# Kernel tuning notes

Hardware: AMD Instinct MI355X
Metric: run time of the kernel (lower is better)

The kernel has to match this reference:

```python
import jax, jax.numpy as jnp
import numpy as np

K = 3          # kernel size
DIL = 1        # dilation
PAD = (K + (K - 1) * (DIL - 1)) // 2   # = 1
CENTER = (K * K - 1) // 2              # = 4
D_MIN = 0.0
D_MAX = 10.0
MIN_NGHBR = 4


def _unfold(x):
    """x: (B,C,H,W) -> patches (B,H,W,k*k,C), matching torch.nn.Unfold ordering."""
    b, c, h, w = x.shape
    xp = jnp.pad(x, ((0, 0), (0, 0), (PAD, PAD), (PAD, PAD)))
    # fixed k*k=9 taps: loop over the kernel window only (not data dims)
    pats = [xp[:, :, i * DIL:i * DIL + h, j * DIL:j * DIL + w]
            for i in range(K) for j in range(K)]
    p = jnp.stack(pats, axis=2)          # (B,C,kk,H,W)
    return p.transpose(0, 3, 4, 2, 1)    # (B,H,W,kk,C)


def setup_inputs() -> dict:
    key = jax.random.key(0)
    kxy, kz = jax.random.split(key)
    B, H, W = 4, 480, 640
    xy = jax.random.normal(kxy, (B, 2, H, W), dtype=jnp.float32)
    z = jax.random.uniform(kz, (B, 1, H, W), dtype=jnp.float32, minval=0.1, maxval=9.9)
    points = jnp.concatenate([xy, z], axis=1)  # (B,3,H,W)
    return {"points": points}


def reference(points):
    b, _, h, w = points.shape
    # 3x3 neighborhoods of 3D points: (B,H,W,9,3)
    A3 = _unfold(points)
    # depth-validity mask, unfolded over the same window: (B,H,W,9,1)
    depth = points[:, 2:3]
    valid = ((depth > D_MIN) & (depth < D_MAX)).astype(points.dtype)
    vc = _unfold(valid)
    # homogeneous design matrix A = [x y z 1], zeroed where neighbor invalid
    A = jnp.concatenate([A3, jnp.ones_like(A3[..., :1])], axis=-1)  # (B,H,W,9,4)
    A = jnp.where(vc > 0.5, A, jnp.zeros_like(A))
    # normal equations: per-pixel symmetric PSD 4x4
    AtA = jnp.einsum('bhwki,bhwkj->bhwij', A, A)
    # A^T A is symmetric PSD -> real eigensystem; eigh gives ascending eigvals,
    # so the null-space direction (smallest eigval) is column 0.
    eig_val, eig_vec = jnp.linalg.eigh(AtA)
    normal4 = eig_vec[..., :, 0]                      # (B,H,W,4)
    normal = normal4[..., :3].transpose(0, 3, 1, 2)   # (B,3,H,W)
    # F.normalize(p=2, dim=1, eps=1e-12)
    nrm = jnp.linalg.norm(normal, axis=1, keepdims=True)
    normal = normal / jnp.maximum(nrm, 1e-12)
    # orient toward the camera ray
    flip = jnp.sign(jnp.sum(normal * points, axis=1, keepdims=True))
    normal = normal * flip
    # validity masks
    vm1 = vc[:, :, :, CENTER, 0][:, None] > 0.5                 # center pixel valid
    vm2 = jnp.sum(vc[..., 0], axis=3)[:, None] >= MIN_NGHBR    # enough neighbors
    # vm3 (real eigensystem) is always True for the symmetric solve
    vm4 = jnp.linalg.norm(normal, axis=1, keepdims=True) > 0.5
    valid_mask = vm1 & vm2 & vm4
    return normal, valid_mask
```

## Files before the change

### kernel.cpp

```cpp
#include <hip/hip_runtime.h>

#define BB 4
#define HH 480
#define WW 640

__device__ __forceinline__ double det3d(double a, double b, double c,
                                        double d, double e, double f,
                                        double g, double h, double i) {
    return a * (e * i - f * h) - b * (d * i - f * g) + c * (d * h - e * g);
}
__device__ __forceinline__ double sdet3d(double a, double b, double c,
                                         double e, double f, double i) {
    return a * (e * i - f * f) + b * (2.0 * c * f - b * i) - c * c * e;
}
__device__ __forceinline__ double crcp(double d) {
    return (double)__builtin_amdgcn_rcpf((float)d);
}
__device__ __forceinline__ float det3f(float a, float b, float c,
                                       float d, float e, float f,
                                       float g, float h, float i) {
    return a * (e * i - f * h) - b * (d * i - f * g) + c * (d * h - e * g);
}
__device__ __forceinline__ float sdet3f(float a, float b, float c,
                                        float e, float f, float i) {
    return a * (e * i - f * f) + b * (2.0f * c * f - b * i) - c * c * e;
}

__global__ __launch_bounds__(256) void d2n_kernel(const float* __restrict__ pts,
                                                  float* __restrict__ out) {
    int idx = blockIdx.x * 256 + threadIdx.x;
    if (idx >= BB * HH * WW) return;
    int x = idx % WW;
    int t1 = idx / WW;
    int y = t1 % HH;
    int b = t1 / HH;

    const size_t HW = (size_t)HH * WW;
    const float* xs = pts + ((size_t)b * 3 + 0) * HW;
    const float* ys = pts + ((size_t)b * 3 + 1) * HW;
    const float* zs = pts + ((size_t)b * 3 + 2) * HW;

    int row[3], col[3];
    bool rin[3], cin[3];
#pragma unroll
    for (int k = 0; k < 3; ++k) {
        int yy = y + k - 1, xx = x + k - 1;
        rin[k] = (unsigned)yy < HH;
        cin[k] = (unsigned)xx < WW;
        row[k] = min(max(yy, 0), HH - 1) * WW;
        col[k] = min(max(xx, 0), WW - 1);
    }
    float px[9], py[9], pz[9];
    bool inb[9];
#pragma unroll
    for (int i = 0; i < 9; ++i) {
        int r = i / 3, c = i % 3;
        int o = row[r] + col[c];
        inb[i] = rin[r] & cin[c];
        pz[i] = zs[o];
        px[i] = xs[o];
        py[i] = ys[o];
    }

    float sxx = 0.f, sxy = 0.f, sxz = 0.f, sx = 0.f;
    float syy = 0.f, syz = 0.f, sy = 0.f;
    float szz = 0.f, sz = 0.f, cnt = 0.f;
#pragma unroll
    for (int i = 0; i < 9; ++i) {
        float w = (inb[i] && pz[i] > 0.0f && pz[i] < 10.0f) ? 1.0f : 0.0f;
        float qx = px[i] * w, qy = py[i] * w, qz = pz[i] * w;
        sxx += qx * px[i]; sxy += qx * py[i]; sxz += qx * pz[i]; sx += qx;
        syy += qy * py[i]; syz += qy * pz[i]; sy += qy;
        szz += qz * pz[i]; sz += qz;
        cnt += w;
    }

    float trf = sxx + syy + szz + cnt;
    float itf = __builtin_amdgcn_rcpf(trf);
    float f00 = sxx * itf, f01 = sxy * itf, f02 = sxz * itf, f03 = sx * itf;
    float f11 = syy * itf, f12 = syz * itf, f13 = sy * itf;
    float f22 = szz * itf, f23 = sz * itf, f33 = cnt * itf;

    float e1f = f00 + f11 + f22 + f33;
    float e2f = (f00 * f11 - f01 * f01) + (f00 * f22 - f02 * f02) +
                (f00 * f33 - f03 * f03) + (f11 * f22 - f12 * f12) +
                (f11 * f33 - f13 * f13) + (f22 * f33 - f23 * f23);
    float Q0 = sdet3f(f11, f12, f13, f22, f23, f33);
    float Q1 = sdet3f(f00, f02, f03, f22, f23, f33);
    float Q2 = sdet3f(f00, f01, f03, f11, f13, f33);
    float Q3 = sdet3f(f00, f01, f02, f11, f12, f22);
    float e3f = Q0 + Q1 + Q2 + Q3;
    float e4f = f00 * Q0
              - f01 * det3f(f01, f12, f13, f02, f22, f23, f03, f23, f33)
              + f02 * det3f(f01, f11, f13, f02, f12, f23, f03, f13, f33)
              - f03 * det3f(f01, f11, f12, f02, f12, f22, f03, f13, f23);

    float t31f = 3.0f * e1f, t22f = 2.0f * e2f;
    float lf = 0.0f;
#pragma unroll
    for (int itn = 0; itn < 10; ++itn) {
        float p  = (((lf - e1f) * lf + e2f) * lf - e3f) * lf + e4f;
        float dp = ((4.0f * lf - t31f) * lf + t22f) * lf - e3f;
        dp = fminf(dp, -1e-30f);
        lf = lf - p * __builtin_amdgcn_rcpf(dp);
        lf = fminf(fmaxf(lf, 0.0f), 0.26f);
    }
    float dpf = ((4.0f * lf - t31f) * lf + t22f) * lf - e3f;

    float g0 = f00 - lf, g1 = f11 - lf, g2 = f22 - lf, g3 = f33 - lf;
    float B00 =  sdet3f(g1, f12, f13, g2, f23, g3);
    float B11 =  sdet3f(g0, f02, f03, g2, f23, g3);
    float B22 =  sdet3f(g0, f01, f03, g1, f13, g3);
    float B33 =  sdet3f(g0, f01, f02, g1, f12, g2);
    float B01 = -det3f(f01, f12, f13, f02, g2, f23, f03, f23, g3);
    float B02 =  det3f(f01, g1, f13, f02, f12, f23, f03, f13, g3);
    float B03 = -det3f(f01, g1, f12, f02, f12, g2, f03, f13, f23);
    float B12 = -det3f(g0, f01, f03, f02, f12, f23, f03, f13, g3);
    float B13 =  det3f(g0, f01, f02, f02, f12, g2, f03, f13, f23);
    float B23 = -det3f(g0, f01, f02, f01, g1, f12, f03, f13, f23);

    float bestf = fabsf(B00);
    float fx = B00, fy = B01, fz = B02;
    float b1a = fabsf(B11);
    if (b1a > bestf) { bestf = b1a; fx = B01; fy = B11; fz = B12; }
    float b2a = fabsf(B22);
    if (b2a > bestf) { bestf = b2a; fx = B02; fy = B12; fz = B22; }
    float b3a = fabsf(B33);
    if (b3a > bestf) { bestf = b3a; fx = B03; fy = B13; fz = B23; }

    float ndf = fx * fx + fy * fy + fz * fz;

    bool flag = !(dpf < -2e-4f) || (lf > 0.2599f) || !(ndf > 1e-12f);

    if (__any(flag)) {
        double tr = (double)sxx + (double)syy + (double)szz + (double)cnt;
        double it = crcp(tr);
        double m00 = sxx * it, m01 = sxy * it, m02 = sxz * it, m03 = sx * it;
        double m11 = syy * it, m12 = syz * it, m13 = sy * it;
        double m22 = szz * it, m23 = sz * it, m33 = cnt * it;

        double e1 = m00 + m11 + m22 + m33;
        double e2 = (m00 * m11 - m01 * m01) + (m00 * m22 - m02 * m02) +
                    (m00 * m33 - m03 * m03) + (m11 * m22 - m12 * m12) +
                    (m11 * m33 - m13 * m13) + (m22 * m33 - m23 * m23);
        double P0 = sdet3d(m11, m12, m13, m22, m23, m33);
        double P1 = sdet3d(m00, m02, m03, m22, m23, m33);
        double P2 = sdet3d(m00, m01, m03, m11, m13, m33);
        double P3 = sdet3d(m00, m01, m02, m11, m12, m22);
        double e3 = P0 + P1 + P2 + P3;
        double e4 = m00 * P0
                  - m01 * det3d(m01, m12, m13, m02, m22, m23, m03, m23, m33)
                  + m02 * det3d(m01, m11, m13, m02, m12, m23, m03, m13, m33)
                  - m03 * det3d(m01, m11, m12, m02, m12, m22, m03, m13, m23);

        double t31 = 3.0 * e1, t22 = 2.0 * e2;
        double lam = 0.0;
#pragma unroll
        for (int itn = 0; itn < 14; ++itn) {
            double p  = (((lam - e1) * lam + e2) * lam - e3) * lam + e4;
            double dp = ((4.0 * lam - t31) * lam + t22) * lam - e3;
            dp = fmin(dp, -1e-30);
            lam = lam - p * crcp(dp);
            lam = fmin(fmax(lam, 0.0), 0.26);
        }

        double d0 = m00 - lam, d1 = m11 - lam, d2 = m22 - lam, d3 = m33 - lam;
        double C00 =  sdet3d(d1, m12, m13, d2, m23, d3);
        double C11 =  sdet3d(d0, m02, m03, d2, m23, d3);
        double C22 =  sdet3d(d0, m01, m03, d1, m13, d3);
        double C33 =  sdet3d(d0, m01, m02, d1, m12, d2);
        double C01 = -det3d(m01, m12, m13, m02, d2, m23, m03, m23, d3);
        double C02 =  det3d(m01, d1, m13, m02, m12, m23, m03, m13, d3);
        double C03 = -det3d(m01, d1, m12, m02, m12, d2, m03, m13, m23);
        double C12 = -det3d(d0, m01, m03, m02, m12, m23, m03, m13, d3);
        double C13 =  det3d(d0, m01, m02, m02, m12, d2, m03, m13, m23);
        double C23 = -det3d(d0, m01, m02, m01, d1, m12, m03, m13, m23);

        double best = fabs(C00);
        double vx = C00, vy = C01, vz = C02, vd = C00;
        double a1 = fabs(C11);
        if (a1 > best) { best = a1; vx = C01; vy = C11; vz = C12; vd = C11; }
        double a2 = fabs(C22);
        if (a2 > best) { best = a2; vx = C02; vy = C12; vz = C22; vd = C22; }
        double a3 = fabs(C33);
        if (a3 > best) { best = a3; vx = C03; vy = C13; vz = C23; vd = C33; }

        double sc = crcp(vd);
        float gx = (float)(vx * sc), gy = (float)(vy * sc), gz = (float)(vz * sc);

        fx = flag ? gx : fx;
        fy = flag ? gy : fy;
        fz = flag ? gz : fz;
        ndf = fx * fx + fy * fy + fz * fz;
    }

    float inv = __builtin_amdgcn_rsqf(fmaxf(ndf, 1e-30f));
    float nx = fx * inv, ny = fy * inv, nz = fz * inv;

    int o = y * WW + x;
    float cx = px[4], cy = py[4], cz = pz[4];
    float dot = nx * cx + ny * cy + nz * cz;
    float sgn = (dot > 0.0f) ? 1.0f : ((dot < 0.0f) ? -1.0f : 0.0f);
    nx *= sgn; ny *= sgn; nz *= sgn;

    out[((size_t)b * 3 + 0) * HW + o] = nx;
    out[((size_t)b * 3 + 1) * HW + o] = ny;
    out[((size_t)b * 3 + 2) * HW + o] = nz;

    bool cvalid = (cz > 0.0f && cz < 10.0f);
    bool m = cvalid && (cnt >= 4.0f) && (nx * nx + ny * ny + nz * nz > 0.25f);
    out[(size_t)BB * 3 * HW + (size_t)b * HW + o] = m ? 1.0f : 0.0f;
}

extern "C" void kernel_launch(void* const* d_in, const int* in_sizes, int n_in,
                              void* d_out, int out_size, void* d_ws, size_t ws_size,
                              hipStream_t stream) {
    const float* pts = (const float*)d_in[0];
    float* out = (float*)d_out;
    int total = BB * HH * WW;
    d2n_kernel<<<(total + 255) / 256, 256, 0, stream>>>(pts, out);
}
```

Measured before the change: 96.87 us.

## Move double-precision fallback into a separate compacted fixup kernel

The main kernel now computes only the float eigenvector path and writes its result for every pixel. Pixels whose float solution looks unreliable are appended to a workspace list through a global atomic counter. A second kernel reloads their neighbourhoods, recomputes the normal in double precision and overwrites the output. This removes the wave-wide divergence where one flagged lane pulled the whole wavefront through the double path. The flag threshold is also loosened so fewer pixels go to the fallback. The cost is a memset, an extra launch, atomic contention on one counter, and possible accuracy loss from the looser threshold.

Result: slower. 206.2 us (+112.9%).

```diff
diff --git a/kernel.cpp b/kernel.cpp
--- a/kernel.cpp
+++ b/kernel.cpp
@@ -3,6 +3,7 @@
 #define BB 4
 #define HH 480
 #define WW 640
+#define NPIX (BB * HH * WW)
 
 __device__ __forceinline__ double det3d(double a, double b, double c,
                                         double d, double e, double f,
@@ -26,20 +27,15 @@
     return a * (e * i - f * f) + b * (2.0f * c * f - b * i) - c * c * e;
 }
 
-__global__ __launch_bounds__(256) void d2n_kernel(const float* __restrict__ pts,
-                                                  float* __restrict__ out) {
-    int idx = blockIdx.x * 256 + threadIdx.x;
-    if (idx >= BB * HH * WW) return;
-    int x = idx % WW;
-    int t1 = idx / WW;
-    int y = t1 % HH;
-    int b = t1 / HH;
-
+__device__ __forceinline__ void load_gram(const float* __restrict__ pts, int x, int y, int b,
+                                          float& sxx, float& sxy, float& sxz, float& sx,
+                                          float& syy, float& syz, float& sy,
+                                          float& szz, float& sz, float& cnt,
+                                          float& cx, float& cy, float& cz) {
     const size_t HW = (size_t)HH * WW;
     const float* xs = pts + ((size_t)b * 3 + 0) * HW;
     const float* ys = pts + ((size_t)b * 3 + 1) * HW;
     const float* zs = pts + ((size_t)b * 3 + 2) * HW;
-
     int row[3], col[3];
     bool rin[3], cin[3];
 #pragma unroll
@@ -61,10 +57,7 @@
         px[i] = xs[o];
         py[i] = ys[o];
     }
-
-    float sxx = 0.f, sxy = 0.f, sxz = 0.f, sx = 0.f;
-    float syy = 0.f, syz = 0.f, sy = 0.f;
-    float szz = 0.f, sz = 0.f, cnt = 0.f;
+    sxx = sxy = sxz = sx = syy = syz = sy = szz = sz = cnt = 0.f;
 #pragma unroll
     for (int i = 0; i < 9; ++i) {
         float w = (inb[i] && pz[i] > 0.0f && pz[i] < 10.0f) ? 1.0f : 0.0f;
@@ -74,6 +67,40 @@
         szz += qz * pz[i]; sz += qz;
         cnt += w;
     }
+    cx = px[4]; cy = py[4]; cz = pz[4];
+}
+
+__device__ __forceinline__ void finish_store(float* __restrict__ out, int x, int y, int b,
+                                             float fx, float fy, float fz,
+                                             float cx, float cy, float cz, float cnt) {
+    const size_t HW = (size_t)HH * WW;
+    float nd = fx * fx + fy * fy + fz * fz;
+    float inv = __builtin_amdgcn_rsqf(fmaxf(nd, 1e-30f));
+    float nx = fx * inv, ny = fy * inv, nz = fz * inv;
+    float dot = nx * cx + ny * cy + nz * cz;
+    float sgn = (dot > 0.0f) ? 1.0f : ((dot < 0.0f) ? -1.0f : 0.0f);
+    nx *= sgn; ny *= sgn; nz *= sgn;
+    int o = y * WW + x;
+    out[((size_t)b * 3 + 0) * HW + o] = nx;
+    out[((size_t)b * 3 + 1) * HW + o] = ny;
+    out[((size_t)b * 3 + 2) * HW + o] = nz;
+    bool cvalid = (cz > 0.0f && cz < 10.0f);
+    bool m = cvalid && (cnt >= 4.0f) && (nx * nx + ny * ny + nz * nz > 0.25f);
+    out[(size_t)BB * 3 * HW + (size_t)b * HW + o] = m ? 1.0f : 0.0f;
+}
+
+__global__ __launch_bounds__(256) void d2n_main(const float* __restrict__ pts,
+                                                float* __restrict__ out,
+                                                int* __restrict__ wslist, int cap) {
+    int idx = blockIdx.x * 256 + threadIdx.x;
+    if (idx >= NPIX) return;
+    int x = idx % WW;
+    int t1 = idx / WW;
+    int y = t1 % HH;
+    int b = t1 / HH;
+
+    float sxx, sxy, sxz, sx, syy, syz, sy, szz, sz, cnt, cx, cy, cz;
+    load_gram(pts, x, y, b, sxx, sxy, sxz, sx, syy, syz, sy, szz, sz, cnt, cx, cy, cz);
 
     float trf = sxx + syy + szz + cnt;
     float itf = __builtin_amdgcn_rcpf(trf);
@@ -130,9 +157,29 @@
 
     float ndf = fx * fx + fy * fy + fz * fz;
 
-    bool flag = !(dpf < -2e-4f) || (lf > 0.2599f) || !(ndf > 1e-12f);
-
-    if (__any(flag)) {
+    bool flag = !(dpf < -2e-5f) || (lf > 0.2599f) || !(ndf > 1e-12f);
+    if (flag) {
+        int slot = atomicAdd(wslist, 1);
+        if (slot < cap) wslist[1 + slot] = idx;
+    }
+
+    finish_store(out, x, y, b, fx, fy, fz, cx, cy, cz, cnt);
+}
+
+__global__ __launch_bounds__(256) void d2n_fixup(const float* __restrict__ pts,
+                                                 float* __restrict__ out,
+                                                 const int* __restrict__ wslist, int cap) {
+    int count = min(wslist[0], cap);
+    for (int i = blockIdx.x * 256 + threadIdx.x; i < count; i += gridDim.x * 256) {
+        int idx = wslist[1 + i];
+        int x = idx % WW;
+        int t1 = idx / WW;
+        int y = t1 % HH;
+        int b = t1 / HH;
+
+        float sxx, sxy, sxz, sx, syy, syz, sy, szz, sz, cnt, cx, cy, cz;
+        load_gram(pts, x, y, b, sxx, sxy, sxz, sx, syy, syz, sy, szz, sz, cnt, cx, cy, cz);
+
         double tr = (double)sxx + (double)syy + (double)szz + (double)cnt;
         double it = crcp(tr);
         double m00 = sxx * it, m01 = sxy * it, m02 = sxz * it, m03 = sx * it;
@@ -186,30 +233,10 @@
         if (a3 > best) { best = a3; vx = C03; vy = C13; vz = C23; vd = C33; }
 
         double sc = crcp(vd);
-        float gx = (float)(vx * sc), gy = (float)(vy * sc), gz = (float)(vz * sc);
-
-        fx = flag ? gx : fx;
-        fy = flag ? gy : fy;
-        fz = flag ? gz : fz;
-        ndf = fx * fx + fy * fy + fz * fz;
-    }
-
-    float inv = __builtin_amdgcn_rsqf(fmaxf(ndf, 1e-30f));
-    float nx = fx * inv, ny = fy * inv, nz = fz * inv;
-
-    int o = y * WW + x;
-    float cx = px[4], cy = py[4], cz = pz[4];
-    float dot = nx * cx + ny * cy + nz * cz;
-    float sgn = (dot > 0.0f) ? 1.0f : ((dot < 0.0f) ? -1.0f : 0.0f);
-    nx *= sgn; ny *= sgn; nz *= sgn;
-
-    out[((size_t)b * 3 + 0) * HW + o] = nx;
-    out[((size_t)b * 3 + 1) * HW + o] = ny;
-    out[((size_t)b * 3 + 2) * HW + o] = nz;
-
-    bool cvalid = (cz > 0.0f && cz < 10.0f);
-    bool m = cvalid && (cnt >= 4.0f) && (nx * nx + ny * ny + nz * nz > 0.25f);
-    out[(size_t)BB * 3 * HW + (size_t)b * HW + o] = m ? 1.0f : 0.0f;
+        float fx = (float)(vx * sc), fy = (float)(vy * sc), fz = (float)(vz * sc);
+
+        finish_store(out, x, y, b, fx, fy, fz, cx, cy, cz, cnt);
+    }
 }
 
 extern "C" void kernel_launch(void* const* d_in, const int* in_sizes, int n_in,
@@ -217,6 +244,10 @@
                               hipStream_t stream) {
     const float* pts = (const float*)d_in[0];
     float* out = (float*)d_out;
-    int total = BB * HH * WW;
-    d2n_kernel<<<(total + 255) / 256, 256, 0, stream>>>(pts, out);
-}
+    int* wslist = (int*)d_ws;
+    int cap = (int)((ws_size / 4 > (size_t)(NPIX + 1)) ? NPIX : (int)(ws_size / 4) - 1);
+
+    hipMemsetAsync(wslist, 0, 4, stream);
+    d2n_main<<<(NPIX + 255) / 256, 256, 0, stream>>>(pts, out, wslist, cap);
+    d2n_fixup<<<64, 256, 0, stream>>>(pts, out, wslist, cap);
+}
```
